# Optimization experiments

Measured on AMD Instinct MI355X. Metric: run time of the kernel, lower is better.

The kernel has to match this reference:

```python
import jax, jax.numpy as jnp
import numpy as np

DIM = 256
HEAD_DIM = 32
HEADS = DIM // HEAD_DIM
SHAPE = (64, 64)          # (H, W) patch grid
WS = 8                    # window size
SHIFT = 4                 # shift size (ws // 2)
SCALE = HEAD_DIM ** -0.5
WS2 = WS * WS


def _rel_indices(ws):
    # relative position index for every (query, key) pair in a window
    a = np.arange(ws)
    y1, x1, y2, x2 = np.meshgrid(a, a, a, a, indexing='ij')
    idx = (y1 - y2 + ws - 1) * (2 * ws - 1) + (x1 - x2 + ws - 1)
    return idx.reshape(ws * ws, ws * ws)  # (ws2, ws2)


def _shift_mask(shape, ws, shift):
    # region labels per patch, 9 regions from the 3x3 slice grid
    H, W = shape
    region = np.zeros((H, W), dtype=np.int32)
    slices = [slice(0, -ws), slice(-ws, -shift), slice(-shift, None)]
    num = 0
    for i in slices:
        for j in slices:
            region[i, j] = num
            num += 1
    # window-partition the region map -> (n_windows, ws2)
    nH, nW = H // ws, W // ws
    r = region.reshape(nH, ws, nW, ws).transpose(0, 2, 1, 3).reshape(nH * nW, ws * ws)
    # True where query and key come from different regions
    return (r[:, None, :] - r[:, :, None]) != 0  # (nw, ws2, ws2)


REL_IDX = jnp.asarray(_rel_indices(WS))                 # (ws2, ws2) int
MASK = jnp.asarray(_shift_mask(SHAPE, WS, SHIFT))       # (nw, ws2, ws2) bool


def _split_windows(x, ws):
    # (b, H, W, C) -> (b * nH * nW, ws*ws, C)
    b, H, W, C = x.shape
    x = x.reshape(b, H // ws, ws, W // ws, ws, C)
    x = x.transpose(0, 1, 3, 2, 4, 5)
    return x.reshape(-1, ws * ws, C)


def _merge_windows(x, shape, ws):
    # inverse of _split_windows
    H, W = shape
    nH, nW = H // ws, W // ws
    C = x.shape[-1]
    x = x.reshape(-1, nH, nW, ws, ws, C)
    x = x.transpose(0, 1, 3, 2, 4, 5)
    return x.reshape(-1, H, W, C)


def setup_inputs() -> dict:
    key = jax.random.key(0)
    ks = jax.random.split(key, 6)
    s = 0.02
    return {
        'x': jax.random.normal(ks[0], (32, SHAPE[0] * SHAPE[1], DIM), jnp.float32),
        'w_qkv': jax.random.normal(ks[1], (3 * DIM, DIM), jnp.float32) * s,
        'b_qkv': jax.random.normal(ks[2], (3 * DIM,), jnp.float32) * s,
        'w_out': jax.random.normal(ks[3], (DIM, DIM), jnp.float32) * s,
        'b_out': jax.random.normal(ks[4], (DIM,), jnp.float32) * s,
        'pos_enc': jax.random.normal(ks[5], (HEADS, (2 * WS - 1) ** 2), jnp.float32) * s,
    }


def reference(x, w_qkv, b_qkv, w_out, b_out, pos_enc):
    B, N, C = x.shape
    H, W = SHAPE
    nw = (H // WS) * (W // WS)

    xg = x.reshape(B, H, W, C)
    if SHIFT > 0:
        xg = jnp.roll(xg, (-SHIFT, -SHIFT), axis=(1, 2))
    xw = _split_windows(xg, WS)                        # (B*nw, ws2, C)

    qkv = xw @ w_qkv.T + b_qkv                         # (B*nw, ws2, 3C)
    qkv = qkv.reshape(-1, WS2, 3, HEADS, HEAD_DIM)
    q, k, v = (qkv[:, :, i].transpose(0, 2, 1, 3) for i in range(3))  # (Bn, h, ws2, hd)

    attn = jnp.einsum('bhqd,bhkd->bhqk', q, k) * SCALE  # (Bn, h, ws2, ws2)
    bias = pos_enc[:, REL_IDX]                          # (h, ws2, ws2)
    attn = attn + bias[None]

    if SHIFT > 0:
        attn = attn.reshape(B, nw, HEADS, WS2, WS2)
        attn = jnp.where(MASK[None, :, None], -jnp.inf, attn)
        attn = attn.reshape(B * nw, HEADS, WS2, WS2)

    attn = jax.nn.softmax(attn, axis=-1)
    out = jnp.einsum('bhqk,bhkd->bhqd', attn, v)        # (Bn, h, ws2, hd)
    out = out.transpose(0, 2, 1, 3).reshape(-1, WS2, C)
    out = out @ w_out.T + b_out                         # (Bn, ws2, C)

    out = _merge_windows(out, SHAPE, WS)                # (B, H, W, C)
    if SHIFT > 0:
        out = jnp.roll(out, (SHIFT, SHIFT), axis=(1, 2))
    return out.reshape(B, N, C)
```

## Files before the change

### kernel.cpp

```cpp
#include <hip/hip_runtime.h>
#include <stdint.h>


typedef short short8 __attribute__((ext_vector_type(8)));
typedef short s16x4 __attribute__((ext_vector_type(4)));
typedef float f32x4 __attribute__((ext_vector_type(4)));

typedef __attribute__((address_space(1))) uint32_t g_u32;
typedef __attribute__((address_space(3))) uint32_t l_u32;

#define SCALE 0.17677669529663687f

__device__ __forceinline__ uint16_t f2bf(float f) {
  union { float f; uint32_t u; } c; c.f = f;
  uint32_t r = c.u + 0x7FFFu + ((c.u >> 16) & 1u);
  return (uint16_t)(r >> 16);
}

__device__ __forceinline__ void g2lds16(const void* g, void* l) {
  __builtin_amdgcn_global_load_lds((const g_u32*)g, (l_u32*)l, 16, 0, 0);
}

__global__ __launch_bounds__(256) void cvtw_kernel(const float* __restrict__ wq,
                                                   const float* __restrict__ wo,
                                                   uint16_t* __restrict__ out) {
  int i = (blockIdx.x * 256 + threadIdx.x) * 8;
  const float* src = (i < 196608) ? (wq + i) : (wo + (i - 196608));
  f32x4 a = *(const f32x4*)src;
  f32x4 b = *(const f32x4*)(src + 4);
  short8 v;
  v[0] = (short)f2bf(a[0]); v[1] = (short)f2bf(a[1]);
  v[2] = (short)f2bf(a[2]); v[3] = (short)f2bf(a[3]);
  v[4] = (short)f2bf(b[0]); v[5] = (short)f2bf(b[1]);
  v[6] = (short)f2bf(b[2]); v[7] = (short)f2bf(b[3]);
  *(short8*)(out + i) = v;
}

__global__ __launch_bounds__(256) void bias_kernel(const float* __restrict__ pe,
                                                   float* __restrict__ bm) {
  int bx = blockIdx.x;
  int wd = bx >> 3, head = bx & 7;
  int hw = wd >> 3, ww = wd & 7;
  int tid = threadIdx.x;
  int kk = tid >> 2, a0 = (tid & 3) * 4;
  int jy = kk >> 3, jx = kk & 7;
  int hj = hw * 8 + jy, xj = ww * 8 + jx;
  int rj = (hj >= 60 ? 2 : (hj >= 56 ? 1 : 0)) * 3 + (xj >= 60 ? 2 : (xj >= 56 ? 1 : 0));
  float* dst = bm + (size_t)bx * 4096 + kk * 64 + a0 * 4;
  for (int aa = 0; aa < 4; ++aa) {
    int a = a0 + aa;
    f32x4 v;
#pragma unroll
    for (int ni = 0; ni < 4; ++ni) {
      int i = ni * 16 + a;
      int iy = i >> 3, ix = i & 7;
      int hi = hw * 8 + iy, xi = ww * 8 + ix;
      int ri = (hi >= 60 ? 2 : (hi >= 56 ? 1 : 0)) * 3 + (xi >= 60 ? 2 : (xi >= 56 ? 1 : 0));
      v[ni] = (ri != rj) ? -1e30f : pe[head * 225 + (iy - jy + 7) * 15 + (ix - jx + 7)];
    }
    *(f32x4*)(dst + aa * 4) = v;
  }
}

__global__ __launch_bounds__(256, 2) void qkv_kernel(
    const float* __restrict__ x, const uint16_t* __restrict__ wq,
    const float* __restrict__ bqkv,
    uint16_t* __restrict__ qws, uint16_t* __restrict__ kws, uint16_t* __restrict__ vws) {
  __shared__ uint16_t sm[40960];
  uint16_t* As = sm;
  uint16_t* Bs = sm + 32768;
  const int tid = threadIdx.x, lane = tid & 63, wv = tid >> 6;
  const int quad = lane >> 4, l15 = lane & 15;
  const int m0 = blockIdx.x * 128;

  {
    const int rl = tid >> 3;
    const int cg = tid & 7;
    for (int pass = 0; pass < 4; ++pass) {
      int row = pass * 32 + rl;
      int token = m0 + row;
      int w = token >> 6, t = token & 63;
      int b = w >> 6, wd = w & 63;
      int h = (wd >> 3) * 8 + (t >> 3);
      int xx = (wd & 7) * 8 + (t & 7);
      const float* sp = x + (size_t)(b * 4096 + (((h + 4) & 63) << 6) + ((xx + 4) & 63)) * 256;
      int psw = (row >> 1) & 3;
#pragma unroll
      for (int j = 0; j < 4; ++j) {
        int c0 = cg * 8 + j * 64;
        f32x4 a = *(const f32x4*)(sp + c0);
        f32x4 d = *(const f32x4*)(sp + c0 + 4);
        short8 v;
        v[0] = (short)f2bf(a[0]); v[1] = (short)f2bf(a[1]);
        v[2] = (short)f2bf(a[2]); v[3] = (short)f2bf(a[3]);
        v[4] = (short)f2bf(d[0]); v[5] = (short)f2bf(d[1]);
        v[6] = (short)f2bf(d[2]); v[7] = (short)f2bf(d[3]);
        int ks = c0 >> 5, g = (c0 >> 3) & 3;
        *(short8*)&As[(ks * 128 + row) * 32 + (g ^ psw) * 8] = v;
      }
    }
  }

  const int c0s = wv * 2, c1s = c0s + 1;
  const int perm = ((lane & 3) ^ ((lane >> 3) & 3)) * 8;
  const int wm = (wv & 1) * 64, wn = (wv >> 1) * 64;
  const int fsw = (quad ^ ((l15 >> 1) & 3)) * 8;
  const int tb = m0 + wm;
  uint16_t* epi = &Bs[wv * 1024];
  f32x4 zero = {0.f, 0.f, 0.f, 0.f};

  for (int nt = 0; nt < 6; ++nt) {
    const int n0 = nt * 128;
    const uint16_t* bp0 = wq + (size_t)(n0 + c0s * 16 + (lane >> 2)) * 256 + perm;
    const uint16_t* bp1 = wq + (size_t)(n0 + c1s * 16 + (lane >> 2)) * 256 + perm;
    g2lds16(bp0, &Bs[c0s * 512]);
    g2lds16(bp1, &Bs[c1s * 512]);

    f32x4 acc[4][4];
#pragma unroll
    for (int mi = 0; mi < 4; ++mi)
#pragma unroll
      for (int ni = 0; ni < 4; ++ni) acc[mi][ni] = zero;

#pragma unroll
    for (int ks = 0; ks < 8; ++ks) {
      __syncthreads();
      if (ks < 7) {
        int nbuf = ((ks + 1) & 1) * 4096;
        g2lds16(bp0 + (ks + 1) * 32, &Bs[nbuf + c0s * 512]);
        g2lds16(bp1 + (ks + 1) * 32, &Bs[nbuf + c1s * 512]);
      }
      int buf = (ks & 1) * 4096;
      short8 af[4], bf[4];
#pragma unroll
      for (int mi = 0; mi < 4; ++mi)
        af[mi] = *(const short8*)&As[(ks * 128 + wm + mi * 16 + l15) * 32 + fsw];
#pragma unroll
      for (int ni = 0; ni < 4; ++ni)
        bf[ni] = *(const short8*)&Bs[buf + (wn + ni * 16 + l15) * 32 + fsw];
#pragma unroll
      for (int mi = 0; mi < 4; ++mi)
#pragma unroll
        for (int ni = 0; ni < 4; ++ni)
          acc[mi][ni] = __builtin_amdgcn_mfma_f32_16x16x32_bf16(af[mi], bf[ni], acc[mi][ni], 0, 0, 0);
    }
    float bq4[4];
#pragma unroll
    for (int ni = 0; ni < 4; ++ni) bq4[ni] = bqkv[n0 + wn + ni * 16 + l15];
    const int ng0 = n0 + wn;
    const int sct = ng0 >> 8;

    if (sct < 2) {
      uint16_t* dst = (sct == 0) ? qws : kws;
#pragma unroll
      for (int mi = 0; mi < 4; ++mi) {
#pragma unroll
        for (int ni = 0; ni < 4; ++ni)
#pragma unroll
          for (int r = 0; r < 4; ++r) {
            int tl = quad * 4 + r, t = mi * 16 + tl;
            int n = ni * 16 + l15;
            epi[tl * 64 + ((((n >> 3) ^ (t & 7)) << 3) | (n & 7))] =
                f2bf(acc[mi][ni][r] + bq4[ni]);
          }
#pragma unroll
        for (int cc = 0; cc < 2; ++cc) {
          int chunk = cc * 64 + lane;
          int trl = chunk >> 3, part = chunk & 7;
          int t = mi * 16 + trl;
          short8 v = *(const short8*)&epi[trl * 64 + ((part ^ (t & 7)) << 3)];
          int tok = tb + t, w = tok >> 6, tt = tok & 63;
          int ng = ng0 + part * 8, hd = (ng >> 5) & 7, d = ng & 31;
          *(short8*)&dst[(size_t)((w * 8 + hd) * 64 + tt) * 32 + d] = v;
        }
      }
    } else {
#pragma unroll
      for (int ni = 0; ni < 4; ++ni) {
        int n = ni * 16 + l15;
#pragma unroll
        for (int mi = 0; mi < 4; ++mi) {
          int t0 = mi * 16 + quad * 4;
          s16x4 pv;
          pv[0] = (short)f2bf(acc[mi][ni][0] + bq4[ni]);
          pv[1] = (short)f2bf(acc[mi][ni][1] + bq4[ni]);
          pv[2] = (short)f2bf(acc[mi][ni][2] + bq4[ni]);
          pv[3] = (short)f2bf(acc[mi][ni][3] + bq4[ni]);
          *(s16x4*)&epi[l15 * 64 + ((((t0 >> 3) ^ (n & 7)) << 3) | (t0 & 7))] = pv;
        }
#pragma unroll
        for (int cc = 0; cc < 2; ++cc) {
          int chunk = cc * 64 + lane;
          int drl = chunk >> 3, part = chunk & 7;
          int dr = ni * 16 + drl;
          short8 v = *(const short8*)&epi[drl * 64 + ((part ^ (dr & 7)) << 3)];
          int ng = ng0 + dr, hd = (ng >> 5) & 7, d = ng & 31;
          int tok = tb + part * 8, w = tok >> 6, t = tok & 63;
          *(short8*)&vws[(size_t)((w * 8 + hd) * 32 + d) * 64 + t] = v;
        }
      }
    }
  }
}

__global__ __launch_bounds__(256) void attn_kernel(
    const uint16_t* __restrict__ qws, const uint16_t* __restrict__ kws,
    const uint16_t* __restrict__ vws, const float* __restrict__ bm,
    uint16_t* __restrict__ ao) {
  __shared__ uint16_t P[4][4096];
  const int tid = threadIdx.x, lane = tid & 63, wv = tid >> 6;
  const int quad = lane >> 4, l15 = lane & 15;
  const int gid = blockIdx.x * 4 + wv;
  const int w = gid >> 3, head = gid & 7;
  const uint16_t* qb = qws + (size_t)(w * 8 + head) * 2048;
  const uint16_t* kb = kws + (size_t)(w * 8 + head) * 2048;
  const uint16_t* vb = vws + (size_t)(w * 8 + head) * 2048;
  const float* bmh = bm + (size_t)((w & 63) * 8 + head) * 4096;
  f32x4 zero = {0.f, 0.f, 0.f, 0.f};

  short8 ak[4], bq[4];
#pragma unroll
  for (int mi = 0; mi < 4; ++mi)
    ak[mi] = *(const short8*)&kb[(mi * 16 + l15) * 32 + quad * 8];
#pragma unroll
  for (int ni = 0; ni < 4; ++ni)
    bq[ni] = *(const short8*)&qb[(ni * 16 + l15) * 32 + quad * 8];

  f32x4 s[4][4];
#pragma unroll
  for (int mi = 0; mi < 4; ++mi)
#pragma unroll
    for (int ni = 0; ni < 4; ++ni)
      s[mi][ni] = __builtin_amdgcn_mfma_f32_16x16x32_bf16(ak[mi], bq[ni], zero, 0, 0, 0);

#pragma unroll
  for (int mi = 0; mi < 4; ++mi)
#pragma unroll
    for (int r = 0; r < 4; ++r) {
      int kk = mi * 16 + quad * 4 + r;
      f32x4 b4 = *(const f32x4*)&bmh[kk * 64 + l15 * 4];
#pragma unroll
      for (int ni = 0; ni < 4; ++ni)
        s[mi][ni][r] = s[mi][ni][r] * SCALE + b4[ni];
    }

#pragma unroll
  for (int ni = 0; ni < 4; ++ni) {
    float mx = s[0][ni][0];
#pragma unroll
    for (int mi = 0; mi < 4; ++mi)
#pragma unroll
      for (int r = 0; r < 4; ++r) mx = fmaxf(mx, s[mi][ni][r]);
    mx = fmaxf(mx, __shfl_xor(mx, 16, 64));
    mx = fmaxf(mx, __shfl_xor(mx, 32, 64));
    float sum = 0.f;
#pragma unroll
    for (int mi = 0; mi < 4; ++mi)
#pragma unroll
      for (int r = 0; r < 4; ++r) {
        float e = __expf(s[mi][ni][r] - mx);
        s[mi][ni][r] = e;
        sum += e;
      }
    sum += __shfl_xor(sum, 16, 64);
    sum += __shfl_xor(sum, 32, 64);
    float inv = 1.f / sum;
#pragma unroll
    for (int mi = 0; mi < 4; ++mi)
#pragma unroll
      for (int r = 0; r < 4; ++r) s[mi][ni][r] *= inv;
  }

  uint16_t* Pw = P[wv];
#pragma unroll
  for (int mi = 0; mi < 4; ++mi)
#pragma unroll
    for (int ni = 0; ni < 4; ++ni)
#pragma unroll
      for (int rp = 0; rp < 2; ++rp) {
        int kk = mi * 16 + quad * 4 + rp * 2;
        int q = ni * 16 + l15;
        uint32_t pk = (uint32_t)f2bf(s[mi][ni][rp * 2]) |
                      ((uint32_t)f2bf(s[mi][ni][rp * 2 + 1]) << 16);
        *(uint32_t*)&Pw[q * 64 + ((((kk >> 3) ^ (q & 7)) << 3) | (kk & 7))] = pk;
      }

  f32x4 o[4][2];
#pragma unroll
  for (int mi = 0; mi < 4; ++mi) { o[mi][0] = zero; o[mi][1] = zero; }
#pragma unroll
  for (int ki = 0; ki < 2; ++ki) {
    short8 vf0 = *(const short8*)&vb[(l15) * 64 + ki * 32 + quad * 8];
    short8 vf1 = *(const short8*)&vb[(16 + l15) * 64 + ki * 32 + quad * 8];
#pragma unroll
    for (int mi = 0; mi < 4; ++mi) {
      int q = mi * 16 + l15;
      short8 pa = *(const short8*)&Pw[q * 64 + (((ki * 4 + quad) ^ (q & 7)) << 3)];
      o[mi][0] = __builtin_amdgcn_mfma_f32_16x16x32_bf16(pa, vf0, o[mi][0], 0, 0, 0);
      o[mi][1] = __builtin_amdgcn_mfma_f32_16x16x32_bf16(pa, vf1, o[mi][1], 0, 0, 0);
    }
  }
#pragma unroll
  for (int mi = 0; mi < 4; ++mi)
#pragma unroll
    for (int ni = 0; ni < 2; ++ni)
#pragma unroll
      for (int r = 0; r < 4; ++r) {
        int t = mi * 16 + quad * 4 + r;
        ao[(size_t)(w * 64 + t) * 256 + head * 32 + ni * 16 + l15] = f2bf(o[mi][ni][r]);
      }
}

__global__ __launch_bounds__(256) void oproj_kernel(
    const uint16_t* __restrict__ aob, const uint16_t* __restrict__ wo,
    const float* __restrict__ bout, float* __restrict__ out) {
  __shared__ uint16_t sm[16384];
  uint16_t* As = sm;
  uint16_t* Bs = sm + 8192;
  const int tid = threadIdx.x, lane = tid & 63, wv = tid >> 6;
  const int quad = lane >> 4, l15 = lane & 15;
  const int n0 = blockIdx.x * 128;
  const int m0 = blockIdx.y * 128;

  const int c0 = wv * 2, c1 = c0 + 1;
  const int perm = ((lane & 3) ^ ((lane >> 3) & 3)) * 8;
  const int fsw = (quad ^ ((l15 >> 1) & 3)) * 8;
  const uint16_t* ap0 = aob + (size_t)(m0 + c0 * 16 + (lane >> 2)) * 256 + perm;
  const uint16_t* ap1 = aob + (size_t)(m0 + c1 * 16 + (lane >> 2)) * 256 + perm;
  const uint16_t* bp0 = wo + (size_t)(n0 + c0 * 16 + (lane >> 2)) * 256 + perm;
  const uint16_t* bp1 = wo + (size_t)(n0 + c1 * 16 + (lane >> 2)) * 256 + perm;

  const int wm = (wv & 1) * 64, wn = (wv >> 1) * 64;
  f32x4 zero = {0.f, 0.f, 0.f, 0.f};
  f32x4 acc[4][4];
#pragma unroll
  for (int mi = 0; mi < 4; ++mi)
#pragma unroll
    for (int ni = 0; ni < 4; ++ni) acc[mi][ni] = zero;

  g2lds16(ap0, &As[c0 * 512]);
  g2lds16(ap1, &As[c1 * 512]);
  g2lds16(bp0, &Bs[c0 * 512]);
  g2lds16(bp1, &Bs[c1 * 512]);

#pragma unroll
  for (int ks = 0; ks < 8; ++ks) {
    __syncthreads();
    if (ks < 7) {
      int nb = ((ks + 1) & 1) * 4096, k0 = (ks + 1) * 32;
      g2lds16(ap0 + k0, &As[nb + c0 * 512]);
      g2lds16(ap1 + k0, &As[nb + c1 * 512]);
      g2lds16(bp0 + k0, &Bs[nb + c0 * 512]);
      g2lds16(bp1 + k0, &Bs[nb + c1 * 512]);
    }
    int buf = (ks & 1) * 4096;
    short8 af[4], bf[4];
#pragma unroll
    for (int mi = 0; mi < 4; ++mi)
      af[mi] = *(const short8*)&As[buf + (wm + mi * 16 + l15) * 32 + fsw];
#pragma unroll
    for (int ni = 0; ni < 4; ++ni)
      bf[ni] = *(const short8*)&Bs[buf + (wn + ni * 16 + l15) * 32 + fsw];
#pragma unroll
    for (int mi = 0; mi < 4; ++mi)
#pragma unroll
      for (int ni = 0; ni < 4; ++ni)
        acc[mi][ni] = __builtin_amdgcn_mfma_f32_16x16x32_bf16(af[mi], bf[ni], acc[mi][ni], 0, 0, 0);
  }

  float bo4[4];
#pragma unroll
  for (int ni = 0; ni < 4; ++ni) bo4[ni] = bout[n0 + wn + ni * 16 + l15];
#pragma unroll
  for (int mi = 0; mi < 4; ++mi) {
    int mb = m0 + wm + mi * 16 + quad * 4;
    int w = mb >> 6, t0 = mb & 63;
    int b = w >> 6, wd = w & 63;
    int hw2 = wd >> 3, ww2 = wd & 7;
#pragma unroll
    for (int r = 0; r < 4; ++r) {
      int t = t0 + r;
      int h = hw2 * 8 + (t >> 3), xx = ww2 * 8 + (t & 7);
      int row = (((h + 4) & 63) << 6) | ((xx + 4) & 63);
      float* op = out + ((size_t)b * 4096 + row) * 256 + n0 + wn;
#pragma unroll
      for (int ni = 0; ni < 4; ++ni) op[ni * 16 + l15] = acc[mi][ni][r] + bo4[ni];
    }
  }
}

extern "C" void kernel_launch(void* const* d_in, const int* in_sizes, int n_in,
                              void* d_out, int out_size, void* d_ws, size_t ws_size,
                              hipStream_t stream) {
  const float* x = (const float*)d_in[0];
  const float* w_qkv = (const float*)d_in[1];
  const float* b_qkv = (const float*)d_in[2];
  const float* w_out = (const float*)d_in[3];
  const float* b_out = (const float*)d_in[4];
  const float* pos_enc = (const float*)d_in[5];
  float* out = (float*)d_out;

  uint8_t* ws = (uint8_t*)d_ws;
  uint16_t* aob = (uint16_t*)(ws);
  uint16_t* wqb = (uint16_t*)(ws + 67108864);
  uint16_t* wob = (uint16_t*)(ws + 67502080);
  float*    bmt = (float*)   (ws + 67633152);
  uint16_t* qws = (uint16_t*)(ws + 76021760);
  uint16_t* kws = (uint16_t*)(ws + 143130624);
  uint16_t* vws = (uint16_t*)(ws + 210239488);

  cvtw_kernel<<<128, 256, 0, stream>>>(w_qkv, w_out, wqb);
  bias_kernel<<<512, 256, 0, stream>>>(pos_enc, bmt);
  qkv_kernel<<<1024, 256, 0, stream>>>(x, wqb, b_qkv, qws, kws, vws);
  attn_kernel<<<4096, 256, 0, stream>>>(qws, kws, vws, bmt, aob);
  oproj_kernel<<<dim3(2, 1024), 256, 0, stream>>>(aob, wob, b_out, out);
}
```

Measured before the change: 391.2 us.

## Load GEMM weight fragments directly from global into registers instead of LDS

```diff
diff --git a/kernel.cpp b/kernel.cpp
--- a/kernel.cpp
+++ b/kernel.cpp
@@ -5,9 +5,6 @@
 typedef short short8 __attribute__((ext_vector_type(8)));
 typedef short s16x4 __attribute__((ext_vector_type(4)));
 typedef float f32x4 __attribute__((ext_vector_type(4)));
-
-typedef __attribute__((address_space(1))) uint32_t g_u32;
-typedef __attribute__((address_space(3))) uint32_t l_u32;
 
 #define SCALE 0.17677669529663687f
 
@@ -15,10 +12,6 @@
   union { float f; uint32_t u; } c; c.f = f;
   uint32_t r = c.u + 0x7FFFu + ((c.u >> 16) & 1u);
   return (uint16_t)(r >> 16);
-}
-
-__device__ __forceinline__ void g2lds16(const void* g, void* l) {
-  __builtin_amdgcn_global_load_lds((const g_u32*)g, (l_u32*)l, 16, 0, 0);
 }
 
 __global__ __launch_bounds__(256) void cvtw_kernel(const float* __restrict__ wq,
@@ -66,12 +59,12 @@
     const float* __restrict__ x, const uint16_t* __restrict__ wq,
     const float* __restrict__ bqkv,
     uint16_t* __restrict__ qws, uint16_t* __restrict__ kws, uint16_t* __restrict__ vws) {
-  __shared__ uint16_t sm[40960];
+  __shared__ uint16_t sm[36864];
   uint16_t* As = sm;
-  uint16_t* Bs = sm + 32768;
   const int tid = threadIdx.x, lane = tid & 63, wv = tid >> 6;
   const int quad = lane >> 4, l15 = lane & 15;
   const int m0 = blockIdx.x * 128;
+  uint16_t* epi = sm + 32768 + wv * 1024;
 
   {
     const int rl = tid >> 3;
@@ -101,20 +94,21 @@
     }
   }
 
-  const int c0s = wv * 2, c1s = c0s + 1;
-  const int perm = ((lane & 3) ^ ((lane >> 3) & 3)) * 8;
   const int wm = (wv & 1) * 64, wn = (wv >> 1) * 64;
   const int fsw = (quad ^ ((l15 >> 1) & 3)) * 8;
   const int tb = m0 + wm;
-  uint16_t* epi = &Bs[wv * 1024];
   f32x4 zero = {0.f, 0.f, 0.f, 0.f};
+
+  __syncthreads();
 
   for (int nt = 0; nt < 6; ++nt) {
     const int n0 = nt * 128;
-    const uint16_t* bp0 = wq + (size_t)(n0 + c0s * 16 + (lane >> 2)) * 256 + perm;
-    const uint16_t* bp1 = wq + (size_t)(n0 + c1s * 16 + (lane >> 2)) * 256 + perm;
-    g2lds16(bp0, &Bs[c0s * 512]);
-    g2lds16(bp1, &Bs[c1s * 512]);
+    const uint16_t* bbase = wq + (size_t)(n0 + wn + l15) * 256 + quad * 8;
+
+    short8 bfr[2][4];
+#pragma unroll
+    for (int ni = 0; ni < 4; ++ni)
+      bfr[0][ni] = *(const short8*)(bbase + ni * 4096);
 
     f32x4 acc[4][4];
 #pragma unroll
@@ -124,26 +118,23 @@
 
 #pragma unroll
     for (int ks = 0; ks < 8; ++ks) {
-      __syncthreads();
+      const int cur = ks & 1;
       if (ks < 7) {
-        int nbuf = ((ks + 1) & 1) * 4096;
-        g2lds16(bp0 + (ks + 1) * 32, &Bs[nbuf + c0s * 512]);
-        g2lds16(bp1 + (ks + 1) * 32, &Bs[nbuf + c1s * 512]);
-      }
-      int buf = (ks & 1) * 4096;
-      short8 af[4], bf[4];
+#pragma unroll
+        for (int ni = 0; ni < 4; ++ni)
+          bfr[cur ^ 1][ni] = *(const short8*)(bbase + ni * 4096 + (ks + 1) * 32);
+      }
+      short8 af[4];
 #pragma unroll
       for (int mi = 0; mi < 4; ++mi)
         af[mi] = *(const short8*)&As[(ks * 128 + wm + mi * 16 + l15) * 32 + fsw];
 #pragma unroll
-      for (int ni = 0; ni < 4; ++ni)
-        bf[ni] = *(const short8*)&Bs[buf + (wn + ni * 16 + l15) * 32 + fsw];
-#pragma unroll
       for (int mi = 0; mi < 4; ++mi)
 #pragma unroll
         for (int ni = 0; ni < 4; ++ni)
-          acc[mi][ni] = __builtin_amdgcn_mfma_f32_16x16x32_bf16(af[mi], bf[ni], acc[mi][ni], 0, 0, 0);
-    }
+          acc[mi][ni] = __builtin_amdgcn_mfma_f32_16x16x32_bf16(af[mi], bfr[cur][ni], acc[mi][ni], 0, 0, 0);
+    }
+
     float bq4[4];
 #pragma unroll
     for (int ni = 0; ni < 4; ++ni) bq4[ni] = bqkv[n0 + wn + ni * 16 + l15];
@@ -314,77 +305,67 @@
 __global__ __launch_bounds__(256) void oproj_kernel(
     const uint16_t* __restrict__ aob, const uint16_t* __restrict__ wo,
     const float* __restrict__ bout, float* __restrict__ out) {
-  __shared__ uint16_t sm[16384];
-  uint16_t* As = sm;
-  uint16_t* Bs = sm + 8192;
   const int tid = threadIdx.x, lane = tid & 63, wv = tid >> 6;
   const int quad = lane >> 4, l15 = lane & 15;
-  const int n0 = blockIdx.x * 128;
-  const int m0 = blockIdx.y * 128;
-
-  const int c0 = wv * 2, c1 = c0 + 1;
-  const int perm = ((lane & 3) ^ ((lane >> 3) & 3)) * 8;
-  const int fsw = (quad ^ ((l15 >> 1) & 3)) * 8;
-  const uint16_t* ap0 = aob + (size_t)(m0 + c0 * 16 + (lane >> 2)) * 256 + perm;
-  const uint16_t* ap1 = aob + (size_t)(m0 + c1 * 16 + (lane >> 2)) * 256 + perm;
-  const uint16_t* bp0 = wo + (size_t)(n0 + c0 * 16 + (lane >> 2)) * 256 + perm;
-  const uint16_t* bp1 = wo + (size_t)(n0 + c1 * 16 + (lane >> 2)) * 256 + perm;
-
+  const int m0 = blockIdx.x * 128;
   const int wm = (wv & 1) * 64, wn = (wv >> 1) * 64;
   f32x4 zero = {0.f, 0.f, 0.f, 0.f};
-  f32x4 acc[4][4];
-#pragma unroll
-  for (int mi = 0; mi < 4; ++mi)
-#pragma unroll
-    for (int ni = 0; ni < 4; ++ni) acc[mi][ni] = zero;
-
-  g2lds16(ap0, &As[c0 * 512]);
-  g2lds16(ap1, &As[c1 * 512]);
-  g2lds16(bp0, &Bs[c0 * 512]);
-  g2lds16(bp1, &Bs[c1 * 512]);
-
-#pragma unroll
-  for (int ks = 0; ks < 8; ++ks) {
-    __syncthreads();
-    if (ks < 7) {
-      int nb = ((ks + 1) & 1) * 4096, k0 = (ks + 1) * 32;
-      g2lds16(ap0 + k0, &As[nb + c0 * 512]);
-      g2lds16(ap1 + k0, &As[nb + c1 * 512]);
-      g2lds16(bp0 + k0, &Bs[nb + c0 * 512]);
-      g2lds16(bp1 + k0, &Bs[nb + c1 * 512]);
-    }
-    int buf = (ks & 1) * 4096;
-    short8 af[4], bf[4];
-#pragma unroll
-    for (int mi = 0; mi < 4; ++mi)
-      af[mi] = *(const short8*)&As[buf + (wm + mi * 16 + l15) * 32 + fsw];
+
+  const uint16_t* abase = aob + (size_t)(m0 + wm + l15) * 256 + quad * 8;
+
+  for (int nt = 0; nt < 2; ++nt) {
+    const uint16_t* bbase = wo + (size_t)(nt * 128 + wn + l15) * 256 + quad * 8;
+
+    short8 afr[2][4], bfr[2][4];
+#pragma unroll
+    for (int mi = 0; mi < 4; ++mi)
+      afr[0][mi] = *(const short8*)(abase + mi * 4096);
 #pragma unroll
     for (int ni = 0; ni < 4; ++ni)
-      bf[ni] = *(const short8*)&Bs[buf + (wn + ni * 16 + l15) * 32 + fsw];
-#pragma unroll
-    for (int mi = 0; mi < 4; ++mi)
-#pragma unroll
-      for (int ni = 0; ni < 4; ++ni)
-        acc[mi][ni] = __builtin_amdgcn_mfma_f32_16x16x32_bf16(af[mi], bf[ni], acc[mi][ni], 0, 0, 0);
-  }
-
-  float bo4[4];
-#pragma unroll
-  for (int ni = 0; ni < 4; ++ni) bo4[ni] = bout[n0 + wn + ni * 16 + l15];
-#pragma unroll
-  for (int mi = 0; mi < 4; ++mi) {
-    int mb = m0 + wm + mi * 16 + quad * 4;
-    int w = mb >> 6, t0 = mb & 63;
-    int b = w >> 6, wd = w & 63;
-    int hw2 = wd >> 3, ww2 = wd & 7;
-#pragma unroll
-    for (int r = 0; r < 4; ++r) {
-      int t = t0 + r;
-      int h = hw2 * 8 + (t >> 3), xx = ww2 * 8 + (t & 7);
-      int row = (((h + 4) & 63) << 6) | ((xx + 4) & 63);
-      float* op = out + ((size_t)b * 4096 + row) * 256 + n0 + wn;
-#pragma unroll
-      for (int ni = 0; ni < 4; ++ni) op[ni * 16 + l15] = acc[mi][ni][r] + bo4[ni];
+      bfr[0][ni] = *(const short8*)(bbase + ni * 4096);
+
+    f32x4 acc[4][4];
+#pragma unroll
+    for (int mi = 0; mi < 4; ++mi)
+#pragma unroll
+      for (int ni = 0; ni < 4; ++ni) acc[mi][ni] = zero;
+
+#pragma unroll
+    for (int ks = 0; ks < 8; ++ks) {
+      const int cur = ks & 1;
+      if (ks < 7) {
+#pragma unroll
+        for (int mi = 0; mi < 4; ++mi)
+          afr[cur ^ 1][mi] = *(const short8*)(abase + mi * 4096 + (ks + 1) * 32);
+#pragma unroll
+        for (int ni = 0; ni < 4; ++ni)
+          bfr[cur ^ 1][ni] = *(const short8*)(bbase + ni * 4096 + (ks + 1) * 32);
+      }
+#pragma unroll
+      for (int mi = 0; mi < 4; ++mi)
+#pragma unroll
+        for (int ni = 0; ni < 4; ++ni)
+          acc[mi][ni] = __builtin_amdgcn_mfma_f32_16x16x32_bf16(afr[cur][mi], bfr[cur][ni], acc[mi][ni], 0, 0, 0);
+    }
+
+    float bo4[4];
+#pragma unroll
+    for (int ni = 0; ni < 4; ++ni) bo4[ni] = bout[nt * 128 + wn + ni * 16 + l15];
+#pragma unroll
+    for (int mi = 0; mi < 4; ++mi) {
+      int mb = m0 + wm + mi * 16 + quad * 4;
+      int w = mb >> 6, t0 = mb & 63;
+      int b = w >> 6, wd = w & 63;
+      int hw2 = wd >> 3, ww2 = wd & 7;
+#pragma unroll
+      for (int r = 0; r < 4; ++r) {
+        int t = t0 + r;
+        int h = hw2 * 8 + (t >> 3), xx = ww2 * 8 + (t & 7);
+        int row = (((h + 4) & 63) << 6) | ((xx + 4) & 63);
+        float* op = out + ((size_t)b * 4096 + row) * 256 + nt * 128 + wn;
+#pragma unroll
+        for (int ni = 0; ni < 4; ++ni) op[ni * 16 + l15] = acc[mi][ni][r] + bo4[ni];
+      }
     }
   }
 }
@@ -413,5 +394,5 @@
   bias_kernel<<<512, 256, 0, stream>>>(pos_enc, bmt);
   qkv_kernel<<<1024, 256, 0, stream>>>(x, wqb, b_qkv, qws, kws, vws);
   attn_kernel<<<4096, 256, 0, stream>>>(qws, kws, vws, bmt, aob);
-  oproj_kernel<<<dim3(2, 1024), 256, 0, stream>>>(aob, wob, b_out, out);
-}
+  oproj_kernel<<<1024, 256, 0, stream>>>(aob, wob, b_out, out);
+}
```

Result: slower. 475.6 us (+21.6%).

## Fuse QKV projection into windowed attention kernel per window-head group

Applied to the files above, without the earlier changes.

```diff
diff --git a/kernel.cpp b/kernel.cpp
--- a/kernel.cpp
+++ b/kernel.cpp
@@ -62,28 +62,30 @@
   }
 }
 
-__global__ __launch_bounds__(256, 2) void qkv_kernel(
+__global__ __launch_bounds__(256, 2) void wattn_kernel(
     const float* __restrict__ x, const uint16_t* __restrict__ wq,
-    const float* __restrict__ bqkv,
-    uint16_t* __restrict__ qws, uint16_t* __restrict__ kws, uint16_t* __restrict__ vws) {
+    const float* __restrict__ bqkv, const float* __restrict__ bm,
+    uint16_t* __restrict__ ao) {
   __shared__ uint16_t sm[40960];
   uint16_t* As = sm;
-  uint16_t* Bs = sm + 32768;
   const int tid = threadIdx.x, lane = tid & 63, wv = tid >> 6;
   const int quad = lane >> 4, l15 = lane & 15;
-  const int m0 = blockIdx.x * 128;
+  const int b = blockIdx.x;
+  const int w = ((b >> 4) << 3) + (b & 7);
+  const int hh = (b >> 3) & 1;
+  const int h = hh * 4 + wv;
+  const int wd = w & 63, bb = w >> 6;
+  f32x4 zero = {0.f, 0.f, 0.f, 0.f};
 
   {
     const int rl = tid >> 3;
     const int cg = tid & 7;
-    for (int pass = 0; pass < 4; ++pass) {
+#pragma unroll
+    for (int pass = 0; pass < 2; ++pass) {
       int row = pass * 32 + rl;
-      int token = m0 + row;
-      int w = token >> 6, t = token & 63;
-      int b = w >> 6, wd = w & 63;
-      int h = (wd >> 3) * 8 + (t >> 3);
-      int xx = (wd & 7) * 8 + (t & 7);
-      const float* sp = x + (size_t)(b * 4096 + (((h + 4) & 63) << 6) + ((xx + 4) & 63)) * 256;
+      int hy = (wd >> 3) * 8 + (row >> 3);
+      int xx = (wd & 7) * 8 + (row & 7);
+      const float* sp = x + (size_t)(bb * 4096 + (((hy + 4) & 63) << 6) + ((xx + 4) & 63)) * 256;
       int psw = (row >> 1) & 3;
 #pragma unroll
       for (int j = 0; j < 4; ++j) {
@@ -96,135 +98,98 @@
         v[4] = (short)f2bf(d[0]); v[5] = (short)f2bf(d[1]);
         v[6] = (short)f2bf(d[2]); v[7] = (short)f2bf(d[3]);
         int ks = c0 >> 5, g = (c0 >> 3) & 3;
-        *(short8*)&As[(ks * 128 + row) * 32 + (g ^ psw) * 8] = v;
-      }
-    }
-  }
-
-  const int c0s = wv * 2, c1s = c0s + 1;
-  const int perm = ((lane & 3) ^ ((lane >> 3) & 3)) * 8;
-  const int wm = (wv & 1) * 64, wn = (wv >> 1) * 64;
-  const int fsw = (quad ^ ((l15 >> 1) & 3)) * 8;
-  const int tb = m0 + wm;
-  uint16_t* epi = &Bs[wv * 1024];
-  f32x4 zero = {0.f, 0.f, 0.f, 0.f};
-
-  for (int nt = 0; nt < 6; ++nt) {
-    const int n0 = nt * 128;
-    const uint16_t* bp0 = wq + (size_t)(n0 + c0s * 16 + (lane >> 2)) * 256 + perm;
-    const uint16_t* bp1 = wq + (size_t)(n0 + c1s * 16 + (lane >> 2)) * 256 + perm;
-    g2lds16(bp0, &Bs[c0s * 512]);
-    g2lds16(bp1, &Bs[c1s * 512]);
-
-    f32x4 acc[4][4];
-#pragma unroll
-    for (int mi = 0; mi < 4; ++mi)
-#pragma unroll
-      for (int ni = 0; ni < 4; ++ni) acc[mi][ni] = zero;
-
-#pragma unroll
-    for (int ks = 0; ks < 8; ++ks) {
-      __syncthreads();
-      if (ks < 7) {
-        int nbuf = ((ks + 1) & 1) * 4096;
-        g2lds16(bp0 + (ks + 1) * 32, &Bs[nbuf + c0s * 512]);
-        g2lds16(bp1 + (ks + 1) * 32, &Bs[nbuf + c1s * 512]);
-      }
-      int buf = (ks & 1) * 4096;
-      short8 af[4], bf[4];
-#pragma unroll
-      for (int mi = 0; mi < 4; ++mi)
-        af[mi] = *(const short8*)&As[(ks * 128 + wm + mi * 16 + l15) * 32 + fsw];
-#pragma unroll
-      for (int ni = 0; ni < 4; ++ni)
-        bf[ni] = *(const short8*)&Bs[buf + (wn + ni * 16 + l15) * 32 + fsw];
-#pragma unroll
-      for (int mi = 0; mi < 4; ++mi)
-#pragma unroll
-        for (int ni = 0; ni < 4; ++ni)
-          acc[mi][ni] = __builtin_amdgcn_mfma_f32_16x16x32_bf16(af[mi], bf[ni], acc[mi][ni], 0, 0, 0);
-    }
-    float bq4[4];
-#pragma unroll
-    for (int ni = 0; ni < 4; ++ni) bq4[ni] = bqkv[n0 + wn + ni * 16 + l15];
-    const int ng0 = n0 + wn;
-    const int sct = ng0 >> 8;
-
-    if (sct < 2) {
-      uint16_t* dst = (sct == 0) ? qws : kws;
+        *(short8*)&As[(ks * 64 + row) * 32 + ((g ^ psw) << 3)] = v;
+      }
+    }
+  }
+
+  const int fsw = (quad ^ ((l15 >> 1) & 3)) << 3;
+  uint16_t* qk = sm + 16384 + wv * 6144;
+
+  const uint16_t* bb0 = wq + (size_t)(h * 32 + l15) * 256 + quad * 8;
+
+  short8 bfr[2][6];
+#pragma unroll
+  for (int ni = 0; ni < 6; ++ni)
+    bfr[0][ni] = *(const short8*)(bb0 + (ni >> 1) * 65536 + (ni & 1) * 4096);
+
+  f32x4 acc[4][6];
+#pragma unroll
+  for (int mi = 0; mi < 4; ++mi)
+#pragma unroll
+    for (int ni = 0; ni < 6; ++ni) acc[mi][ni] = zero;
+
+  __syncthreads();
+
+#pragma unroll
+  for (int ks = 0; ks < 8; ++ks) {
+    const int cur = ks & 1;
+    if (ks < 7) {
+#pragma unroll
+      for (int ni = 0; ni < 6; ++ni)
+        bfr[cur ^ 1][ni] = *(const short8*)(bb0 + (ni >> 1) * 65536 + (ni & 1) * 4096 + (ks + 1) * 32);
+    }
+    short8 af[4];
+#pragma unroll
+    for (int mi = 0; mi < 4; ++mi)
+      af[mi] = *(const short8*)&As[(ks * 64 + mi * 16 + l15) * 32 + fsw];
+#pragma unroll
+    for (int mi = 0; mi < 4; ++mi)
+#pragma unroll
+      for (int ni = 0; ni < 6; ++ni)
+        acc[mi][ni] = __builtin_amdgcn_mfma_f32_16x16x32_bf16(af[mi], bfr[cur][ni], acc[mi][ni], 0, 0, 0);
+  }
+
+  float bqv[6];
+#pragma unroll
+  for (int ni = 0; ni < 6; ++ni)
+    bqv[ni] = bqkv[(ni >> 1) * 256 + h * 32 + (ni & 1) * 16 + l15];
+
+#pragma unroll
+  for (int ni = 0; ni < 4; ++ni) {
+    uint16_t* dst = qk + (ni >> 1) * 2048;
+    int d = (ni & 1) * 16 + l15, dg = d >> 3;
+#pragma unroll
+    for (int mi = 0; mi < 4; ++mi)
+#pragma unroll
+      for (int r = 0; r < 4; ++r) {
+        int t = mi * 16 + quad * 4 + r;
+        dst[t * 32 + (((dg ^ ((t >> 1) & 3)) << 3) | (d & 7))] =
+            f2bf(acc[mi][ni][r] + bqv[ni]);
+      }
+  }
+  {
+    uint16_t* vdst = qk + 4096;
+#pragma unroll
+    for (int ni = 4; ni < 6; ++ni) {
+      int d = (ni - 4) * 16 + l15;
 #pragma unroll
       for (int mi = 0; mi < 4; ++mi) {
-#pragma unroll
-        for (int ni = 0; ni < 4; ++ni)
-#pragma unroll
-          for (int r = 0; r < 4; ++r) {
-            int tl = quad * 4 + r, t = mi * 16 + tl;
-            int n = ni * 16 + l15;
-            epi[tl * 64 + ((((n >> 3) ^ (t & 7)) << 3) | (n & 7))] =
-                f2bf(acc[mi][ni][r] + bq4[ni]);
-          }
-#pragma unroll
-        for (int cc = 0; cc < 2; ++cc) {
-          int chunk = cc * 64 + lane;
-          int trl = chunk >> 3, part = chunk & 7;
-          int t = mi * 16 + trl;
-          short8 v = *(const short8*)&epi[trl * 64 + ((part ^ (t & 7)) << 3)];
-          int tok = tb + t, w = tok >> 6, tt = tok & 63;
-          int ng = ng0 + part * 8, hd = (ng >> 5) & 7, d = ng & 31;
-          *(short8*)&dst[(size_t)((w * 8 + hd) * 64 + tt) * 32 + d] = v;
-        }
-      }
-    } else {
-#pragma unroll
-      for (int ni = 0; ni < 4; ++ni) {
-        int n = ni * 16 + l15;
-#pragma unroll
-        for (int mi = 0; mi < 4; ++mi) {
-          int t0 = mi * 16 + quad * 4;
-          s16x4 pv;
-          pv[0] = (short)f2bf(acc[mi][ni][0] + bq4[ni]);
-          pv[1] = (short)f2bf(acc[mi][ni][1] + bq4[ni]);
-          pv[2] = (short)f2bf(acc[mi][ni][2] + bq4[ni]);
-          pv[3] = (short)f2bf(acc[mi][ni][3] + bq4[ni]);
-          *(s16x4*)&epi[l15 * 64 + ((((t0 >> 3) ^ (n & 7)) << 3) | (t0 & 7))] = pv;
-        }
-#pragma unroll
-        for (int cc = 0; cc < 2; ++cc) {
-          int chunk = cc * 64 + lane;
-          int drl = chunk >> 3, part = chunk & 7;
-          int dr = ni * 16 + drl;
-          short8 v = *(const short8*)&epi[drl * 64 + ((part ^ (dr & 7)) << 3)];
-          int ng = ng0 + dr, hd = (ng >> 5) & 7, d = ng & 31;
-          int tok = tb + part * 8, w = tok >> 6, t = tok & 63;
-          *(short8*)&vws[(size_t)((w * 8 + hd) * 32 + d) * 64 + t] = v;
-        }
-      }
-    }
-  }
-}
-
-__global__ __launch_bounds__(256) void attn_kernel(
-    const uint16_t* __restrict__ qws, const uint16_t* __restrict__ kws,
-    const uint16_t* __restrict__ vws, const float* __restrict__ bm,
-    uint16_t* __restrict__ ao) {
-  __shared__ uint16_t P[4][4096];
-  const int tid = threadIdx.x, lane = tid & 63, wv = tid >> 6;
-  const int quad = lane >> 4, l15 = lane & 15;
-  const int gid = blockIdx.x * 4 + wv;
-  const int w = gid >> 3, head = gid & 7;
-  const uint16_t* qb = qws + (size_t)(w * 8 + head) * 2048;
-  const uint16_t* kb = kws + (size_t)(w * 8 + head) * 2048;
-  const uint16_t* vb = vws + (size_t)(w * 8 + head) * 2048;
-  const float* bmh = bm + (size_t)((w & 63) * 8 + head) * 4096;
-  f32x4 zero = {0.f, 0.f, 0.f, 0.f};
+        int t0 = mi * 16 + quad * 4;
+        s16x4 pv;
+        pv[0] = (short)f2bf(acc[mi][ni][0] + bqv[ni]);
+        pv[1] = (short)f2bf(acc[mi][ni][1] + bqv[ni]);
+        pv[2] = (short)f2bf(acc[mi][ni][2] + bqv[ni]);
+        pv[3] = (short)f2bf(acc[mi][ni][3] + bqv[ni]);
+        *(s16x4*)&vdst[d * 64 + (t0 ^ ((d & 7) << 3))] = pv;
+      }
+    }
+  }
+
+  __syncthreads();
+
+  const uint16_t* qb2 = qk;
+  const uint16_t* kb2 = qk + 2048;
+  const uint16_t* vb2 = qk + 4096;
+  const float* bmh = bm + ((size_t)wd * 8 + h) * 4096;
 
   short8 ak[4], bq[4];
 #pragma unroll
   for (int mi = 0; mi < 4; ++mi)
-    ak[mi] = *(const short8*)&kb[(mi * 16 + l15) * 32 + quad * 8];
+    ak[mi] = *(const short8*)&kb2[(mi * 16 + l15) * 32 + fsw];
 #pragma unroll
   for (int ni = 0; ni < 4; ++ni)
-    bq[ni] = *(const short8*)&qb[(ni * 16 + l15) * 32 + quad * 8];
+    bq[ni] = *(const short8*)&qb2[(ni * 16 + l15) * 32 + fsw];
 
   f32x4 s[4][4];
 #pragma unroll
@@ -271,7 +236,7 @@
       for (int r = 0; r < 4; ++r) s[mi][ni][r] *= inv;
   }
 
-  uint16_t* Pw = P[wv];
+  uint16_t* Pw = sm + wv * 4096;
 #pragma unroll
   for (int mi = 0; mi < 4; ++mi)
 #pragma unroll
@@ -290,8 +255,9 @@
   for (int mi = 0; mi < 4; ++mi) { o[mi][0] = zero; o[mi][1] = zero; }
 #pragma unroll
   for (int ki = 0; ki < 2; ++ki) {
-    short8 vf0 = *(const short8*)&vb[(l15) * 64 + ki * 32 + quad * 8];
-    short8 vf1 = *(const short8*)&vb[(16 + l15) * 64 + ki * 32 + quad * 8];
+    int tc = ki * 32 + quad * 8;
+    short8 vf0 = *(const short8*)&vb2[l15 * 64 + (tc ^ ((l15 & 7) << 3))];
+    short8 vf1 = *(const short8*)&vb2[(16 + l15) * 64 + (tc ^ ((l15 & 7) << 3))];
 #pragma unroll
     for (int mi = 0; mi < 4; ++mi) {
       int q = mi * 16 + l15;
@@ -307,7 +273,7 @@
 #pragma unroll
       for (int r = 0; r < 4; ++r) {
         int t = mi * 16 + quad * 4 + r;
-        ao[(size_t)(w * 64 + t) * 256 + head * 32 + ni * 16 + l15] = f2bf(o[mi][ni][r]);
+        ao[(size_t)(w * 64 + t) * 256 + h * 32 + ni * 16 + l15] = f2bf(o[mi][ni][r]);
       }
 }
 
@@ -405,13 +371,9 @@
   uint16_t* wqb = (uint16_t*)(ws + 67108864);
   uint16_t* wob = (uint16_t*)(ws + 67502080);
   float*    bmt = (float*)   (ws + 67633152);
-  uint16_t* qws = (uint16_t*)(ws + 76021760);
-  uint16_t* kws = (uint16_t*)(ws + 143130624);
-  uint16_t* vws = (uint16_t*)(ws + 210239488);
 
   cvtw_kernel<<<128, 256, 0, stream>>>(w_qkv, w_out, wqb);
   bias_kernel<<<512, 256, 0, stream>>>(pos_enc, bmt);
-  qkv_kernel<<<1024, 256, 0, stream>>>(x, wqb, b_qkv, qws, kws, vws);
-  attn_kernel<<<4096, 256, 0, stream>>>(qws, kws, vws, bmt, aob);
+  wattn_kernel<<<4096, 256, 0, stream>>>(x, wqb, b_qkv, bmt, aob);
   oproj_kernel<<<dim3(2, 1024), 256, 0, stream>>>(aob, wob, b_out, out);
 }
```

After: 367.7 us. 6.0% less time.
